# Performance work log

Hardware: AMD Instinct MI355X
Metric: run time of the kernel (lower is better)

The kernel has to match this reference:

```python
import jax, jax.numpy as jnp
import numpy as np

PATCH = 3
ALPHA = 0.1


def _unfold3x3(x):
    # x: [B, C, H, W] -> [B, C*9, H, W], torch F.unfold with k=3, pad=1, stride=1
    B, C, H, W = x.shape
    p = PATCH // 2
    xp = jnp.pad(x, ((0, 0), (0, 0), (p, p), (p, p)))
    shifts = [xp[:, :, i:i + H, j:j + W] for i in range(PATCH) for j in range(PATCH)]
    # torch unfold orders (C, kh, kw); ordering is irrelevant for the dot-product
    # correlation, but we match it anyway: stack kernel positions after channel.
    out = jnp.stack(shifts, axis=2)  # [B, C, 9, H, W]
    return out.reshape(B, C * PATCH * PATCH, H, W)


def setup_inputs() -> dict:
    key = jax.random.key(0)
    k1, k2 = jax.random.split(key)
    x_lab = jax.random.normal(k1, (4, 3, 64, 64), dtype=jnp.float32)
    feature = jax.random.normal(k2, (4, 64, 64, 64), dtype=jnp.float32)
    return {"x_lab": x_lab, "feature": feature}


def reference(x_lab, feature):
    # scale_factor=1 and feature already at (H, W): both interpolates are identity.
    B, _, H, W = x_lab.shape
    N = H * W
    x_ab = x_lab.reshape(B, 3, N).transpose(0, 2, 1)          # [B, N, 3]
    lf = _unfold3x3(feature).reshape(B, -1, N)                 # [B, C*9, N]
    corr = jnp.einsum('bcn,bcm->bnm', lf, lf)                  # [B, N, N]
    attn = jax.nn.softmax(corr / ALPHA, axis=-1)
    weighted = jnp.einsum('bnm,bmc->bnc', attn, x_ab)          # [B, N, 3]
    return weighted.transpose(0, 2, 1).reshape(B, 3, H, W)
```

## Files before the change

kernel.cpp:

```cpp
#include <hip/hip_runtime.h>


#define NPIX 4096
#define ROWB  (528 * 16)
#define SCALE 10.0f
#define XCH   1024

typedef __attribute__((ext_vector_type(8))) short bf16x8;
typedef __attribute__((ext_vector_type(4))) float f32x4;

#define MF(a, b, c) __builtin_amdgcn_mfma_f32_16x16x32_bf16(a, b, c, 0, 0, 0)

__device__ __forceinline__ float blo(unsigned u) { return __uint_as_float(u << 16); }
__device__ __forceinline__ float bhi(unsigned u) { return __uint_as_float(u & 0xffff0000u); }

#define MG(T, DBASE, KT) do {                                                 \
    _Pragma("unroll")                                                         \
    for (int dx = 0; dx < 3; ++dx)                                            \
        _Pragma("unroll")                                                     \
        for (int ks = 0; ks < 2; ++ks)                                        \
            acc[T][KT] = MF(AF[((DBASE) + dx) * 2 + ks], B2[ks][dx], acc[T][KT]); \
} while (0)

#define RETIRE(S, myv) do {                                                   \
    _Pragma("unroll")                                                         \
    for (int kt = 0; kt < 4; ++kt) {                                          \
        const int kx = kt * 16 + nl;                                          \
        const float xv0 = xls[(myv) * 64 + kx];                               \
        const float xv1 = xls[XCH + (myv) * 64 + kx];                         \
        const float xv2 = xls[2 * XCH + (myv) * 64 + kx];                     \
        _Pragma("unroll")                                                     \
        for (int rg = 0; rg < 4; ++rg) {                                      \
            const float e = __expf(fmaf(acc[S][kt][rg], SCALE, negM[rg]));    \
            l_[rg] += e;                                                      \
            A0[rg] = fmaf(e, xv0, A0[rg]);                                    \
            A1[rg] = fmaf(e, xv1, A1[rg]);                                    \
            A2[rg] = fmaf(e, xv2, A2[rg]);                                    \
        }                                                                     \
        acc[S][kt] = (f32x4){0.f, 0.f, 0.f, 0.f};                             \
    }                                                                         \
} while (0)

#define STEP(RM, SN, SR, tt) do {                                             \
    const int t_ = (tt);                                                      \
    uint4 Rv0 = (uint4){0u, 0u, 0u, 0u}, Rv1 = (uint4){0u, 0u, 0u, 0u};       \
    if (t_ <= 15) {                                                           \
        const int g2 = R0 + 1 + t_;                                           \
        if (g2 < 64) {                                                        \
            Rv0 = fbb[kc0 * NPIX + g2 * 64 + x];                              \
            Rv1 = fbb[kc1 * NPIX + g2 * 64 + x];                              \
        }                                                                     \
    }                                                                         \
    {                                                                         \
        const char* base = ring + (RM) * ROWB + bu;                           \
        _Pragma("unroll")                                                     \
        for (int kt = 0; kt < 4; ++kt) {                                      \
            bf16x8 B2[2][3];                                                  \
            _Pragma("unroll")                                                 \
            for (int ks = 0; ks < 2; ++ks) {                                  \
                const char* p = base + (ks * 264 + kt * 16) * 16;             \
                B2[ks][0] = *(const bf16x8*)(p);                              \
                B2[ks][1] = *(const bf16x8*)(p + 16);                         \
                B2[ks][2] = *(const bf16x8*)(p + 32);                         \
            }                                                                 \
            if (t_ >= 2)              MG(((SR)), 6, kt);    \
            if (t_ >= 1 && t_ <= 16)  MG(((RM)), 3, kt);    \
            if (t_ <= 15)             MG(((SN)), 0, kt);    \
        }                                                                     \
    }                                                                         \
    if (t_ >= 2) RETIRE(SR, t_ - 2);                                          \
    if (t_ <= 15) {                                                           \
        *(uint4*)(ring + (SR) * ROWB + wu0) = Rv0;                            \
        *(uint4*)(ring + (SR) * ROWB + wu1) = Rv1;                            \
    }                                                                         \
    if (t_ < 17) __syncthreads();                                             \
} while (0)

__global__ __launch_bounds__(256)
void nlwa_convert(const float* __restrict__ feature, uint4* __restrict__ fb)
{
    const int idx = blockIdx.x * 256 + threadIdx.x;
    const int p = idx & (NPIX - 1);
    const int cb = idx >> 12;
    const float* src = feature + (size_t)cb * 8 * NPIX + p;
    unsigned h[8];
#pragma unroll
    for (int j = 0; j < 8; ++j) {
        unsigned u = __float_as_uint(src[(size_t)j * NPIX]);
        u = u + 0x7fffu + ((u >> 16) & 1u);
        h[j] = u >> 16;
    }
    fb[idx] = (uint4){h[0] | (h[1] << 16), h[2] | (h[3] << 16),
                      h[4] | (h[5] << 16), h[6] | (h[7] << 16)};
}

__global__ __launch_bounds__(256)
__attribute__((amdgpu_waves_per_eu(2)))
void nlwa_fused(const float* __restrict__ x_lab,
                const uint4* __restrict__ fb16,
                float4* __restrict__ ws)
{
    __shared__ __align__(16) char ring[3 * ROWB];
    __shared__ float xls[3 * XCH];
    __shared__ float part[3][4][64];
    __shared__ float ssq[3][64];

    const int tid = threadIdx.x;
    const int b = blockIdx.x >> 8;
    const int rem = blockIdx.x & 255;
    const int ny = rem >> 2, kq = rem & 3;
    const int R0 = kq * 16;
    const int w = tid >> 6, lane = tid & 63;
    const int quad = lane >> 4, nl = lane & 15;
    const int kc0 = 2 * w, kc1 = 2 * w + 1;
    const int x = lane;
    const int wu0 = (kc0 * 66 + x + 1) * 16;
    const int wu1 = (kc1 * 66 + x + 1) * 16;
    const int bu = (quad * 66 + nl) * 16;

    const uint4* fbb = fb16 + (size_t)b * 8 * NPIX;
    const float* xb = x_lab + (size_t)b * 3 * NPIX;

    {
        const int base = R0 * 64;
        float4* d4 = (float4*)xls;
        for (int i = tid; i < 3 * XCH / 4; i += 256) {
            const int ch = i >> 8, off = i & 255;
            d4[i] = *(const float4*)(xb + (size_t)ch * NPIX + base + off * 4);
        }
    }
    if (tid < 48) {
        const int sl = tid / 16, pu = tid % 16;
        const int u = (pu >> 1) * 66 + (pu & 1) * 65;
        *(uint4*)(ring + sl * ROWB + u * 16) = (uint4){0u, 0u, 0u, 0u};
    }

#pragma unroll
    for (int dyi = 0; dyi < 3; ++dyi) {
        const int qr = ny + dyi - 1;
        float ss = 0.f;
        if (qr >= 0 && qr < 64) {
            const uint4 v0 = fbb[kc0 * NPIX + qr * 64 + x];
            const uint4 v1 = fbb[kc1 * NPIX + qr * 64 + x];
            const unsigned* pv0 = (const unsigned*)&v0;
            const unsigned* pv1 = (const unsigned*)&v1;
#pragma unroll
            for (int d = 0; d < 4; ++d) {
                float a0 = blo(pv0[d]), a1 = bhi(pv0[d]);
                float b0 = blo(pv1[d]), b1 = bhi(pv1[d]);
                ss = fmaf(a0, a0, ss); ss = fmaf(a1, a1, ss);
                ss = fmaf(b0, b0, ss); ss = fmaf(b1, b1, ss);
            }
        }
        part[dyi][w][x] = ss;
    }

    bf16x8 AF[18];
#pragma unroll
    for (int dyi = 0; dyi < 3; ++dyi) {
        const int qr = ny + dyi - 1;
#pragma unroll
        for (int dx = 0; dx < 3; ++dx) {
            const int cxx = w * 16 + nl + dx - 1;
#pragma unroll
            for (int ks = 0; ks < 2; ++ks) {
                bf16x8 t = (bf16x8){0, 0, 0, 0, 0, 0, 0, 0};
                if (qr >= 0 && qr < 64 && cxx >= 0 && cxx < 64)
                    t = *(const bf16x8*)(fbb + (quad + 4 * ks) * NPIX + qr * 64 + cxx);
                AF[(dyi * 3 + dx) * 2 + ks] = t;
            }
        }
    }

#pragma unroll
    for (int rr = 0; rr < 2; ++rr) {
        const int g = R0 - 1 + rr;
        uint4 v0 = (uint4){0u, 0u, 0u, 0u}, v1 = v0;
        if (g >= 0) {
            v0 = fbb[kc0 * NPIX + g * 64 + x];
            v1 = fbb[kc1 * NPIX + g * 64 + x];
        }
        *(uint4*)(ring + rr * ROWB + wu0) = v0;
        *(uint4*)(ring + rr * ROWB + wu1) = v1;
    }
    __syncthreads();

    if (tid < 192) {
        const int dyi = tid >> 6, xx = tid & 63;
        float s = 0.f;
#pragma unroll
        for (int k = 0; k < 4; ++k) s += part[dyi][k][xx];
        ssq[dyi][xx] = s;
    }
    __syncthreads();

    float negM[4];
#pragma unroll
    for (int rg = 0; rg < 4; ++rg) {
        const int q = w * 16 + quad * 4 + rg;
        float a = 0.f;
#pragma unroll
        for (int dyi = 0; dyi < 3; ++dyi)
#pragma unroll
            for (int dx = -1; dx <= 1; ++dx) {
                const int cx = q + dx;
                a += (cx >= 0 && cx < 64) ? ssq[dyi][cx] : 0.f;
            }
        negM[rg] = -SCALE * a;
    }

    float l_[4], A0[4], A1[4], A2[4];
#pragma unroll
    for (int rg = 0; rg < 4; ++rg) { l_[rg] = 0.f; A0[rg] = 0.f; A1[rg] = 0.f; A2[rg] = 0.f; }
    f32x4 acc[3][4];
#pragma unroll
    for (int i = 0; i < 3; ++i)
#pragma unroll
        for (int kt = 0; kt < 4; ++kt)
            acc[i][kt] = (f32x4){0.f, 0.f, 0.f, 0.f};

    for (int rb = 0; rb < 18; rb += 3) {
        STEP(0, 1, 2, rb);
        STEP(1, 2, 0, rb + 1);
        STEP(2, 0, 1, rb + 2);
    }

#pragma unroll
    for (int rg = 0; rg < 4; ++rg) {
#pragma unroll
        for (int off = 8; off >= 1; off >>= 1) {
            l_[rg] += __shfl_down(l_[rg], off, 16);
            A0[rg] += __shfl_down(A0[rg], off, 16);
            A1[rg] += __shfl_down(A1[rg], off, 16);
            A2[rg] += __shfl_down(A2[rg], off, 16);
        }
    }
    if (nl == 0) {
#pragma unroll
        for (int rg = 0; rg < 4; ++rg) {
            const int q = w * 16 + quad * 4 + rg;
            ws[(size_t)blockIdx.x * 64 + q] =
                make_float4(l_[rg], A0[rg], A1[rg], A2[rg]);
        }
    }
}

__global__ __launch_bounds__(256)
void nlwa_combine(const float4* __restrict__ ws, float* __restrict__ out)
{
    const int i = blockIdx.x * 256 + threadIdx.x;
    const int b = i >> 12, ny = (i >> 6) & 63, q = i & 63;
    const size_t base = ((size_t)(b * 64 + ny) * 4) * 64 + q;
    float4 s = make_float4(0.f, 0.f, 0.f, 0.f);
#pragma unroll
    for (int kq = 0; kq < 4; ++kq) {
        const float4 p = ws[base + (size_t)kq * 64];
        s.x += p.x; s.y += p.y; s.z += p.z; s.w += p.w;
    }
    const float inv = 1.0f / s.x;
    float* o = out + (size_t)b * 3 * NPIX + ny * 64 + q;
    o[0]        = s.y * inv;
    o[NPIX]     = s.z * inv;
    o[2 * NPIX] = s.w * inv;
}

extern "C" void kernel_launch(void* const* d_in, const int* in_sizes, int n_in,
                              void* d_out, int out_size, void* d_ws, size_t ws_size,
                              hipStream_t stream) {
    (void)in_sizes; (void)n_in; (void)out_size; (void)ws_size;
    const float* x_lab   = (const float*)d_in[0];
    const float* feature = (const float*)d_in[1];
    float* out = (float*)d_out;
    float4* wsp = (float4*)d_ws;
    uint4* fb   = (uint4*)((char*)d_ws + (1 << 20));
    nlwa_convert<<<dim3(512), dim3(256), 0, stream>>>(feature, fb);
    nlwa_fused<<<dim3(1024), dim3(256), 0, stream>>>(x_lab, fb, wsp);
    nlwa_combine<<<dim3(64), dim3(256), 0, stream>>>(wsp, out);
}
```

Measured before the change: 127.9 us.

## Use four-slot LDS ring to halve block barriers per row step

```diff
diff --git a/kernel.cpp b/kernel.cpp
--- a/kernel.cpp
+++ b/kernel.cpp
@@ -41,18 +41,17 @@
     }                                                                         \
 } while (0)
 
-#define STEP(RM, SN, SR, tt) do {                                             \
-    const int t_ = (tt);                                                      \
+#define STEPX(TT) do {                                                        \
     uint4 Rv0 = (uint4){0u, 0u, 0u, 0u}, Rv1 = (uint4){0u, 0u, 0u, 0u};       \
-    if (t_ <= 15) {                                                           \
-        const int g2 = R0 + 1 + t_;                                           \
+    if ((TT) <= 15) {                                                         \
+        const int g2 = R0 + 1 + (TT);                                         \
         if (g2 < 64) {                                                        \
             Rv0 = fbb[kc0 * NPIX + g2 * 64 + x];                              \
             Rv1 = fbb[kc1 * NPIX + g2 * 64 + x];                              \
         }                                                                     \
     }                                                                         \
     {                                                                         \
-        const char* base = ring + (RM) * ROWB + bu;                           \
+        const char* base = ring + ((TT) % 4) * ROWB + bu;                     \
         _Pragma("unroll")                                                     \
         for (int kt = 0; kt < 4; ++kt) {                                      \
             bf16x8 B2[2][3];                                                  \
@@ -63,17 +62,23 @@
                 B2[ks][1] = *(const bf16x8*)(p + 16);                         \
                 B2[ks][2] = *(const bf16x8*)(p + 32);                         \
             }                                                                 \
-            if (t_ >= 2)              MG(((SR)), 6, kt);    \
-            if (t_ >= 1 && t_ <= 16)  MG(((RM)), 3, kt);    \
-            if (t_ <= 15)             MG(((SN)), 0, kt);    \
+            if ((TT) >= 2)                MG(((TT) + 2) % 3, 6, kt);          \
+            if ((TT) >= 1 && (TT) <= 16)  MG((TT) % 3,       3, kt);          \
+            if ((TT) <= 15)               MG(((TT) + 1) % 3, 0, kt);          \
         }                                                                     \
     }                                                                         \
-    if (t_ >= 2) RETIRE(SR, t_ - 2);                                          \
-    if (t_ <= 15) {                                                           \
-        *(uint4*)(ring + (SR) * ROWB + wu0) = Rv0;                            \
-        *(uint4*)(ring + (SR) * ROWB + wu1) = Rv1;                            \
-    }                                                                         \
-    if (t_ < 17) __syncthreads();                                             \
+    if ((TT) >= 2) RETIRE(((TT) + 2) % 3, (TT) - 2);                          \
+    if ((TT) <= 15) {                                                         \
+        *(uint4*)(ring + (((TT) + 2) % 4) * ROWB + wu0) = Rv0;                \
+        *(uint4*)(ring + (((TT) + 2) % 4) * ROWB + wu1) = Rv1;                \
+    }                                                                         \
+} while (0)
+
+#define S2(TT) do {                                                           \
+    STEPX(TT);                                                                \
+    __builtin_amdgcn_sched_barrier(0);                                        \
+    STEPX((TT) + 1);                                                          \
+    if ((TT) < 16) __syncthreads();                                           \
 } while (0)
 
 __global__ __launch_bounds__(256)
@@ -100,7 +105,7 @@
                 const uint4* __restrict__ fb16,
                 float4* __restrict__ ws)
 {
-    __shared__ __align__(16) char ring[3 * ROWB];
+    __shared__ __align__(16) char ring[4 * ROWB];
     __shared__ float xls[3 * XCH];
     __shared__ float part[3][4][64];
     __shared__ float ssq[3][64];
@@ -129,7 +134,7 @@
             d4[i] = *(const float4*)(xb + (size_t)ch * NPIX + base + off * 4);
         }
     }
-    if (tid < 48) {
+    if (tid < 64) {
         const int sl = tid / 16, pu = tid % 16;
         const int u = (pu >> 1) * 66 + (pu & 1) * 65;
         *(uint4*)(ring + sl * ROWB + u * 16) = (uint4){0u, 0u, 0u, 0u};
@@ -219,11 +224,8 @@
         for (int kt = 0; kt < 4; ++kt)
             acc[i][kt] = (f32x4){0.f, 0.f, 0.f, 0.f};
 
-    for (int rb = 0; rb < 18; rb += 3) {
-        STEP(0, 1, 2, rb);
-        STEP(1, 2, 0, rb + 1);
-        STEP(2, 0, 1, rb + 2);
-    }
+    S2(0);  S2(2);  S2(4);  S2(6);  S2(8);
+    S2(10); S2(12); S2(14); S2(16);
 
 #pragma unroll
     for (int rg = 0; rg < 4; ++rg) {
```

New measurement: 273.6 us. 2.14x slower.
